# Kernel optimization log

Hardware: AMD Instinct MI355X
Metric: run time of the kernel (lower is better)

The kernel has to match this reference:

```python
import jax, jax.numpy as jnp
import numpy as np

B, S, D, H = 2, 2048, 1024, 8
DH = D // H          # hidden_dim == attn_dim == 128
TOTAL = 4 * D        # (2*hidden_dim + 2*attn_dim) * H
EPS = 1e-5
ROPE_BASE = 10000.0


def _layernorm(x, g, b):
    m = jnp.mean(x, axis=-1, keepdims=True)
    v = jnp.mean(jnp.square(x - m), axis=-1, keepdims=True)
    return (x - m) * jax.lax.rsqrt(v + EPS) * g + b


def _rope(x):
    # x: [B, H, S, DH], interleaved even/odd RoPE as in the torch module
    half = DH // 2
    inv_freq = 1.0 / (ROPE_BASE ** (jnp.arange(0, DH, 2, dtype=jnp.float32) / DH))  # [half]
    t = jnp.arange(x.shape[2], dtype=jnp.float32)
    freqs = t[:, None] * inv_freq[None, :]                 # [S, half]
    cos = jnp.cos(freqs)[None, None, :, :]                 # [1,1,S,half]
    sin = jnp.sin(freqs)[None, None, :, :]
    xe, xo = x[..., 0::2], x[..., 1::2]
    re = xe * cos - xo * sin
    ro = xe * sin + xo * cos
    return jnp.stack([re, ro], axis=-1).reshape(x.shape)


def setup_inputs() -> dict:
    key = jax.random.key(0)
    ks = jax.random.split(key, 6)
    x = jax.random.normal(ks[0], (B, S, D), dtype=jnp.float32)
    attention_mask = jnp.ones((B, S), dtype=bool)
    # weights stored [in, out] so forward is x @ W + b
    w_uvqk = 0.02 * jax.random.normal(ks[1], (D, TOTAL), dtype=jnp.float32)
    b_uvqk = jnp.zeros((TOTAL,), dtype=jnp.float32)
    w_out = 0.02 * jax.random.normal(ks[2], (3 * D, D), dtype=jnp.float32)
    b_out = jnp.zeros((D,), dtype=jnp.float32)
    ln1_g = jnp.ones((D,), dtype=jnp.float32)
    ln1_b = jnp.zeros((D,), dtype=jnp.float32)
    ln2_g = jnp.ones((D,), dtype=jnp.float32)
    ln2_b = jnp.zeros((D,), dtype=jnp.float32)
    return {"x": x, "attention_mask": attention_mask,
            "ln1_g": ln1_g, "ln1_b": ln1_b,
            "w_uvqk": w_uvqk, "b_uvqk": b_uvqk,
            "ln2_g": ln2_g, "ln2_b": ln2_b,
            "w_out": w_out, "b_out": b_out}


def reference(x, attention_mask, ln1_g, ln1_b, w_uvqk, b_uvqk, ln2_g, ln2_b, w_out, b_out):
    normed = _layernorm(x, ln1_g, ln1_b)
    uvqk = jax.nn.silu(normed @ w_uvqk + b_uvqk)          # [B,S,4D]
    u, v, q, k = jnp.split(uvqk, [D, 2 * D, 3 * D], axis=-1)
    q = q.reshape(B, S, H, DH).transpose(0, 2, 1, 3)      # [B,H,S,DH]
    k = k.reshape(B, S, H, DH).transpose(0, 2, 1, 3)
    v = v.reshape(B, S, H, DH).transpose(0, 2, 1, 3)
    q, k = _rope(q), _rope(k)
    scale = jnp.float32(DH) ** 0.5
    scores = jnp.einsum('bhsd,bhtd->bhst', q, k) / scale  # [B,H,S,S] fp32
    causal = jnp.tril(jnp.ones((S, S), dtype=bool))
    pad = attention_mask[:, None, :, None] & attention_mask[:, None, None, :]
    valid = pad & causal[None, None, :, :]
    scores = jnp.where(valid, scores, jnp.float32(-30.0))
    scores = jnp.clip(scores, -30.0, 30.0)
    attn = jax.nn.silu(scores)                            # SiLU instead of softmax
    ao = jnp.einsum('bhst,bhtd->bhsd', attn, v)           # [B,H,S,DH]
    ao = ao.transpose(0, 2, 1, 3).reshape(B, S, D)
    normed_attn = _layernorm(ao, ln2_g, ln2_b)
    cat = jnp.concatenate([u, ao, normed_attn * u], axis=-1)  # [B,S,3D]
    return x + (cat @ w_out + b_out)
```

## Files before the change

kernel.cpp:

```cpp
#include <hip/hip_runtime.h>
#include <hip/hip_bf16.h>
#include <math.h>

#define Bm 2
#define Sm 2048
#define Dm 1024
#define Hm 8
#define DHm 128
#define TOTALm 4096
#define ROWS (Bm*Sm)
#define K2m (3*Dm)

typedef __bf16 bf16;
typedef __bf16 bf16x8 __attribute__((ext_vector_type(8)));
typedef __bf16 bf16x4 __attribute__((ext_vector_type(4)));
typedef float  f32x4  __attribute__((ext_vector_type(4)));

__device__ __forceinline__ void stage_tile_128x32(
    const bf16* __restrict__ g, int ld, bf16* lds, int tid)
{
    int wid = tid >> 6;
    #pragma unroll
    for (int j = 0; j < 2; j++) {
        int e0  = (j*256 + tid) * 8;
        int row = e0 >> 5, col = e0 & 31;
        const bf16* src = g + (size_t)row*ld + col;
        bf16* dst = lds + (size_t)(j*256 + wid*64)*8;
        __builtin_amdgcn_global_load_lds(
            (const __attribute__((address_space(1))) unsigned int*)src,
            (__attribute__((address_space(3))) unsigned int*)dst,
            16, 0, 0);
    }
}

__device__ __forceinline__ void stage_tile_64x32(
    const bf16* __restrict__ g, int ld, bf16* lds, int tid)
{
    int wid = tid >> 6;
    int e0 = tid * 8;
    int row = e0 >> 5, col = e0 & 31;
    const bf16* src = g + (size_t)row*ld + col;
    bf16* dst = lds + (size_t)wid*512;
    __builtin_amdgcn_global_load_lds(
        (const __attribute__((address_space(1))) unsigned int*)src,
        (__attribute__((address_space(3))) unsigned int*)dst,
        16, 0, 0);
}

__global__ __launch_bounds__(256) void prep_kernel(
    const float* __restrict__ x, const float* __restrict__ g1,
    const float* __restrict__ b1, bf16* __restrict__ normed,
    const float* __restrict__ w_uvqk, bf16* __restrict__ Wt1,
    const float* __restrict__ w_out,  bf16* __restrict__ Wt2,
    float* __restrict__ ct, float* __restrict__ st)
{
    __shared__ float tile[32][33];
    __shared__ float red[4];
    __shared__ float stats[2];
    int bid = blockIdx.x;
    int tid = threadIdx.x;
    if (bid < 7168) {
        const float* in; bf16* out; int R, C, bx, by;
        if (bid < 4096) { in = w_uvqk; out = Wt1; R = Dm;  C = TOTALm; bx = bid & 127; by = bid >> 7; }
        else { int id2 = bid - 4096; in = w_out; out = Wt2; R = K2m; C = Dm; bx = id2 & 31; by = id2 >> 5; }
        int c0 = bx*32, r0 = by*32;
        int tx = tid & 31, ty = tid >> 5;
        for (int i=0;i<4;i++) {
            int r = ty + i*8;
            tile[r][tx] = in[(size_t)(r0+r)*C + c0+tx];
        }
        __syncthreads();
        for (int i=0;i<4;i++) {
            int cl = ty + i*8;
            out[(size_t)(c0+cl)*R + r0+tx] = (bf16)tile[tx][cl];
        }
    } else if (bid < 7680) {
        int idx = (bid - 7168)*256 + tid;
        int t = idx >> 6, p = idx & 63;
        float inv = expf(-0.143911568f * (float)p);
        float f = (float)t * inv;
        float sv, cv;
        sincosf(f, &sv, &cv);
        ct[idx] = cv; st[idx] = sv;
    } else {
        int row = bid - 7680;
        const float* xr = x + (size_t)row * Dm;
        float4 v = *(const float4*)(xr + tid*4);
        float s = v.x+v.y+v.z+v.w;
        for (int o=32;o>0;o>>=1) s += __shfl_down(s,o);
        int wid = tid>>6, lane = tid&63;
        if (lane==0) red[wid]=s;
        __syncthreads();
        if (tid==0) stats[0] = (red[0]+red[1]+red[2]+red[3]) * (1.f/Dm);
        __syncthreads();
        float m = stats[0];
        float d0=v.x-m,d1=v.y-m,d2=v.z-m,d3=v.w-m;
        float q = d0*d0+d1*d1+d2*d2+d3*d3;
        for (int o=32;o>0;o>>=1) q += __shfl_down(q,o);
        if (lane==0) red[wid]=q;
        __syncthreads();
        if (tid==0) stats[1] = rsqrtf((red[0]+red[1]+red[2]+red[3])*(1.f/Dm) + 1e-5f);
        __syncthreads();
        float rs = stats[1];
        float4 gv = *(const float4*)(g1 + tid*4);
        float4 bv = *(const float4*)(b1 + tid*4);
        bf16x4 o;
        o[0] = (bf16)(d0*rs*gv.x + bv.x);
        o[1] = (bf16)(d1*rs*gv.y + bv.y);
        o[2] = (bf16)(d2*rs*gv.z + bv.z);
        o[3] = (bf16)(d3*rs*gv.w + bv.w);
        *(bf16x4*)(normed + (size_t)row*Dm + tid*4) = o;
    }
}

__global__ __launch_bounds__(256,4) void gemm1_kernel(
    const bf16* __restrict__ A, const bf16* __restrict__ Bt,
    const float* __restrict__ bias,
    const float* __restrict__ ct, const float* __restrict__ st,
    bf16* __restrict__ cat, bf16* __restrict__ qb, bf16* __restrict__ kb,
    bf16* __restrict__ vt)
{
    __shared__ __align__(16) bf16 sm[17408];
    const int K = Dm;
    int m0 = blockIdx.y*128, n0 = blockIdx.x*128;
    int tid = threadIdx.x, wid = tid>>6, lane = tid&63;
    int quad = lane>>4, l16 = lane&15;
    int wm = (wid>>1)*64, wn = (wid&1)*64;
    f32x4 acc[4][4] = {};
    bf16* sA = sm;
    bf16* sB = sm + 8192;
    for (int k0=0;k0<K;k0+=64) {
        __syncthreads();
        stage_tile_128x32(A  + (size_t)m0*K + k0,      K, sA,        tid);
        stage_tile_128x32(A  + (size_t)m0*K + k0 + 32, K, sA + 4096, tid);
        stage_tile_128x32(Bt + (size_t)n0*K + k0,      K, sB,        tid);
        stage_tile_128x32(Bt + (size_t)n0*K + k0 + 32, K, sB + 4096, tid);
        __syncthreads();
        #pragma unroll
        for (int kc=0;kc<2;kc++) {
            bf16x8 af[4], bfr[4];
            #pragma unroll
            for (int t=0;t<4;t++) af[t]  = *(const bf16x8*)&sA[kc*4096 + (wm+t*16+l16)*32 + quad*8];
            #pragma unroll
            for (int t=0;t<4;t++) bfr[t] = *(const bf16x8*)&sB[kc*4096 + (wn+t*16+l16)*32 + quad*8];
            #pragma unroll
            for (int tm=0;tm<4;tm++)
                #pragma unroll
                for (int tn=0;tn<4;tn++)
                    acc[tm][tn] = __builtin_amdgcn_mfma_f32_16x16x32_bf16(af[tm], bfr[tn], acc[tm][tn], 0,0,0);
        }
    }
    int sect = n0 >> 10;
    if (sect == 1) {
        __syncthreads();
        #pragma unroll
        for (int tm=0;tm<4;tm++)
        #pragma unroll
        for (int tn=0;tn<4;tn++) {
            int colg = n0 + wn + tn*16 + l16;
            float bval = bias[colg];
            int d = colg & 127;
            #pragma unroll
            for (int r=0;r<4;r++) {
                int srow = wm + tm*16 + quad*4 + r;
                float val = acc[tm][tn][r] + bval;
                val = val / (1.f + __expf(-val));
                sm[d*136 + srow] = (bf16)val;
            }
        }
        __syncthreads();
        int h = (n0 >> 7) & 7;
        int b = m0 >> 11, s0l = m0 & 2047;
        int d2 = tid >> 1, sh = (tid & 1)*64;
        bf16* dst = vt + ((size_t)(b*Hm+h)*DHm + d2)*Sm + s0l + sh;
        const bf16* srcl = &sm[d2*136 + sh];
        #pragma unroll
        for (int i=0;i<8;i++)
            *(bf16x8*)(dst + i*8) = *(const bf16x8*)(srcl + i*8);
    } else if (sect == 0) {
        #pragma unroll
        for (int tm=0;tm<4;tm++)
        #pragma unroll
        for (int tn=0;tn<4;tn++) {
            int c = n0 + wn + tn*16 + l16;
            float bval = bias[c];
            #pragma unroll
            for (int r=0;r<4;r++) {
                int row = m0 + wm + tm*16 + quad*4 + r;
                float val = acc[tm][tn][r] + bval;
                val = val / (1.f + __expf(-val));
                cat[(size_t)row*K2m + c] = (bf16)val;
            }
        }
    } else {
        bf16* dstb = (sect==2) ? qb : kb;
        float postscale = (sect==2) ? 0.08838834764831845f : 1.0f;
        #pragma unroll
        for (int tm=0;tm<4;tm++)
        #pragma unroll
        for (int tn=0;tn<4;tn++) {
            int colg = n0 + wn + tn*16 + l16;
            int c = colg & 1023;
            int h = c>>7, d = c&127, p = d>>1;
            float bval = bias[colg];
            #pragma unroll
            for (int r=0;r<4;r++) {
                int row = m0 + wm + tm*16 + quad*4 + r;
                float val = acc[tm][tn][r] + bval;
                val = val / (1.f + __expf(-val));
                int b = row>>11, s = row&2047;
                float pv = __shfl_xor(val, 1);
                float cv = ct[s*64+p], sv = st[s*64+p];
                float res = (d&1) ? (pv*sv + val*cv) : (val*cv - pv*sv);
                dstb[((size_t)(b*Hm+h)*Sm + s)*DHm + d] = (bf16)(res * postscale);
            }
        }
    }
}

__global__ __launch_bounds__(256,3) void attn_kernel(
    const bf16* __restrict__ qb, const bf16* __restrict__ kb,
    const bf16* __restrict__ vt, float* __restrict__ ao0,
    float* __restrict__ ao1)
{
    __shared__ __align__(16) bf16 sK[16384];
    __shared__ __align__(16) bf16 P[64*136];
    int bid = blockIdx.x;
    int head = bid & 15;
    int idx = bid >> 4;
    int b = head >> 3, h = head & 7;
    int qt, k_begin, k_end;
    float* aoOut;
    if (idx < 32) {
        qt = 31 - (idx >> 1);
        int nkt = (qt >> 1) + 1;
        int half = (nkt + 1) >> 1;
        if ((idx & 1) == 0) { k_begin = 0;    k_end = half; aoOut = ao0; }
        else                { k_begin = half; k_end = nkt;  aoOut = ao1; }
    } else {
        qt = idx - 32;
        k_begin = 0; k_end = (qt >> 1) + 1;
        aoOut = ao0;
    }
    const size_t headoff = (size_t)(b*Hm+h)*Sm*DHm;
    const bf16* Q  = qb + headoff;
    const bf16* Km = kb + headoff;
    const bf16* V  = vt + headoff;
    int tid=threadIdx.x, wid=tid>>6, lane=tid&63, quad=lane>>4, l16=lane&15;
    int wm=(wid>>1)*32, wn=(wid&1)*64;
    int q0 = qt*64;
    f32x4 accO[2][4] = {};
    bf16x8 qf[4][2];
    #pragma unroll
    for (int kc=0;kc<4;kc++)
        #pragma unroll
        for (int t=0;t<2;t++)
            qf[kc][t] = *(const bf16x8*)(Q + (size_t)(q0+wm+t*16+l16)*DHm + kc*32 + quad*8);
    int e0 = tid*8, e1 = (256+tid)*8;
    int kr0 = e0>>5, kcol0 = e0&31;
    int kr1 = e1>>5, kcol1 = e1&31;
    int xorv = (tid>>3)&3;
    int sw0 = kr0*32 + (((tid&3)^xorv)<<3);
    int sw1 = sw0 + 2048;
    bf16x8 kreg[4][2];
    {
        int t0 = k_begin*128;
        #pragma unroll
        for (int kc=0;kc<4;kc++) {
            kreg[kc][0] = *(const bf16x8*)(Km + (size_t)(t0+kr0)*DHm + kc*32 + kcol0);
            kreg[kc][1] = *(const bf16x8*)(Km + (size_t)(t0+kr1)*DHm + kc*32 + kcol1);
        }
    }
    for (int kt=k_begin; kt<k_end; kt++) {
        int t0 = kt*128;
        __syncthreads();
        #pragma unroll
        for (int kc=0;kc<4;kc++) {
            *(bf16x8*)&sK[kc*4096 + sw0] = kreg[kc][0];
            *(bf16x8*)&sK[kc*4096 + sw1] = kreg[kc][1];
        }
        __syncthreads();
        if (kt+1 < k_end) {
            int t0n = t0 + 128;
            #pragma unroll
            for (int kc=0;kc<4;kc++) {
                kreg[kc][0] = *(const bf16x8*)(Km + (size_t)(t0n+kr0)*DHm + kc*32 + kcol0);
                kreg[kc][1] = *(const bf16x8*)(Km + (size_t)(t0n+kr1)*DHm + kc*32 + kcol1);
            }
        }
        bool clean = (t0 + 127 <= q0);
        #pragma unroll
        for (int ts=0; ts<4; ts++) {
            f32x4 accS[2] = {};
            int rr = wn + ts*16 + l16;
            int csw = (quad ^ ((rr>>1)&3))<<3;
            #pragma unroll
            for (int kc=0;kc<4;kc++) {
                bf16x8 bfr = *(const bf16x8*)&sK[kc*4096 + rr*32 + csw];
                #pragma unroll
                for (int tm=0;tm<2;tm++)
                    accS[tm] = __builtin_amdgcn_mfma_f32_16x16x32_bf16(qf[kc][tm], bfr, accS[tm], 0,0,0);
            }
            #pragma unroll
            for (int tm=0;tm<2;tm++)
                #pragma unroll
                for (int r=0;r<4;r++) {
                    int srow = wm+tm*16+quad*4+r;
                    float s = fminf(30.f, accS[tm][r]);
                    float p = s * __builtin_amdgcn_rcpf(1.f + __expf(-s));
                    if (!clean && (t0+rr > q0+srow)) p = 0.f;
                    P[srow*136 + rr] = (bf16)p;
                }
        }
        __syncthreads();
        int kcn = ((q0 + 63 - t0) >> 5) + 1;
        if (kcn > 4) kcn = 4;
        for (int kc=0;kc<kcn;kc++) {
            bf16x8 af[2], bfr[4];
            #pragma unroll
            for (int t=0;t<2;t++) af[t]  = *(const bf16x8*)&P[(wm+t*16+l16)*136 + kc*32 + quad*8];
            #pragma unroll
            for (int t=0;t<4;t++) bfr[t] = *(const bf16x8*)(V + (size_t)(wn+t*16+l16)*Sm + t0 + kc*32 + quad*8);
            #pragma unroll
            for (int tm=0;tm<2;tm++)
                #pragma unroll
                for (int tn=0;tn<4;tn++)
                    accO[tm][tn] = __builtin_amdgcn_mfma_f32_16x16x32_bf16(af[tm], bfr[tn], accO[tm][tn], 0,0,0);
        }
    }
    #pragma unroll
    for (int tm=0;tm<2;tm++)
    #pragma unroll
    for (int tn=0;tn<4;tn++)
        #pragma unroll
        for (int r=0;r<4;r++) {
            int s = q0+wm+tm*16+quad*4+r;
            int d = wn+tn*16+l16;
            aoOut[((size_t)(b*Sm+s))*Dm + h*DHm + d] = accO[tm][tn][r];
        }
}

__global__ __launch_bounds__(256) void ln2_cat_kernel(
    const float* __restrict__ ao0, const float* __restrict__ ao1,
    const float* __restrict__ g,
    const float* __restrict__ bb, bf16* __restrict__ cat)
{
    int row = blockIdx.x;
    int tid = threadIdx.x;
    int s = row & 2047;
    float4 v  = *(const float4*)(ao0 + (size_t)row*Dm + tid*4);
    if (s >= 1024) {
        float4 v1 = *(const float4*)(ao1 + (size_t)row*Dm + tid*4);
        v.x += v1.x; v.y += v1.y; v.z += v1.z; v.w += v1.w;
    }
    float ssum = v.x+v.y+v.z+v.w;
    for (int o=32;o>0;o>>=1) ssum += __shfl_down(ssum,o);
    __shared__ float red[4]; __shared__ float stats[2];
    int wid = tid>>6, lane = tid&63;
    if (lane==0) red[wid]=ssum;
    __syncthreads();
    if (tid==0) stats[0] = (red[0]+red[1]+red[2]+red[3]) * (1.f/Dm);
    __syncthreads();
    float m = stats[0];
    float d0=v.x-m,d1=v.y-m,d2=v.z-m,d3=v.w-m;
    float q = d0*d0+d1*d1+d2*d2+d3*d3;
    for (int o=32;o>0;o>>=1) q += __shfl_down(q,o);
    if (lane==0) red[wid]=q;
    __syncthreads();
    if (tid==0) stats[1] = rsqrtf((red[0]+red[1]+red[2]+red[3])*(1.f/Dm) + 1e-5f);
    __syncthreads();
    float rs = stats[1];
    float4 gv = *(const float4*)(g + tid*4);
    float4 bv = *(const float4*)(bb + tid*4);
    bf16* crow = cat + (size_t)row * K2m;
    bf16x4 u4 = *(const bf16x4*)(crow + tid*4);
    bf16x4 a4, nu4;
    a4[0]=(bf16)v.x; a4[1]=(bf16)v.y; a4[2]=(bf16)v.z; a4[3]=(bf16)v.w;
    nu4[0]=(bf16)(((v.x-m)*rs*gv.x+bv.x) * (float)u4[0]);
    nu4[1]=(bf16)(((v.y-m)*rs*gv.y+bv.y) * (float)u4[1]);
    nu4[2]=(bf16)(((v.z-m)*rs*gv.z+bv.z) * (float)u4[2]);
    nu4[3]=(bf16)(((v.w-m)*rs*gv.w+bv.w) * (float)u4[3]);
    *(bf16x4*)(crow + 1024 + tid*4) = a4;
    *(bf16x4*)(crow + 2048 + tid*4) = nu4;
}

__global__ __launch_bounds__(256,4) void gemm2_kernel(
    const bf16* __restrict__ A, const bf16* __restrict__ Bt,
    const float* __restrict__ bias, const float* __restrict__ x,
    float* __restrict__ out)
{
    __shared__ __align__(16) bf16 sm[12288];
    const int K = K2m, N = Dm;
    int m0 = blockIdx.y*128, n0 = blockIdx.x*64;
    int tid = threadIdx.x, wid = tid>>6, lane = tid&63;
    int quad = lane>>4, l16 = lane&15;
    int wm = (wid>>1)*64, wn = (wid&1)*32;
    f32x4 acc[4][2] = {};
    bf16* sA = sm;
    bf16* sB = sm + 8192;
    for (int k0=0;k0<K;k0+=64) {
        __syncthreads();
        stage_tile_128x32(A  + (size_t)m0*K + k0,      K, sA,        tid);
        stage_tile_128x32(A  + (size_t)m0*K + k0 + 32, K, sA + 4096, tid);
        stage_tile_64x32 (Bt + (size_t)n0*K + k0,      K, sB,        tid);
        stage_tile_64x32 (Bt + (size_t)n0*K + k0 + 32, K, sB + 2048, tid);
        __syncthreads();
        #pragma unroll
        for (int kc=0;kc<2;kc++) {
            bf16x8 af[4], bfr[2];
            #pragma unroll
            for (int t=0;t<4;t++) af[t]  = *(const bf16x8*)&sA[kc*4096 + (wm+t*16+l16)*32 + quad*8];
            #pragma unroll
            for (int t=0;t<2;t++) bfr[t] = *(const bf16x8*)&sB[kc*2048 + (wn+t*16+l16)*32 + quad*8];
            #pragma unroll
            for (int tm=0;tm<4;tm++)
                #pragma unroll
                for (int tn=0;tn<2;tn++)
                    acc[tm][tn] = __builtin_amdgcn_mfma_f32_16x16x32_bf16(af[tm], bfr[tn], acc[tm][tn], 0,0,0);
        }
    }
    #pragma unroll
    for (int tm=0;tm<4;tm++)
    #pragma unroll
    for (int tn=0;tn<2;tn++) {
        int col = n0 + wn + tn*16 + l16;
        float bval = bias[col];
        #pragma unroll
        for (int r=0;r<4;r++) {
            int row = m0 + wm + tm*16 + quad*4 + r;
            out[(size_t)row*N + col] = acc[tm][tn][r] + bval + x[(size_t)row*N + col];
        }
    }
}

extern "C" void kernel_launch(void* const* d_in, const int* in_sizes, int n_in,
                              void* d_out, int out_size, void* d_ws, size_t ws_size,
                              hipStream_t stream)
{
    const float* x      = (const float*)d_in[0];
    const float* ln1_g  = (const float*)d_in[2];
    const float* ln1_b  = (const float*)d_in[3];
    const float* w_uvqk = (const float*)d_in[4];
    const float* b_uvqk = (const float*)d_in[5];
    const float* ln2_g  = (const float*)d_in[6];
    const float* ln2_b  = (const float*)d_in[7];
    const float* w_out  = (const float*)d_in[8];
    const float* b_out  = (const float*)d_in[9];

    char* w = (char*)d_ws;
    bf16*  normed = (bf16*)(w);
    bf16*  Wt1    = (bf16*)(w + 8388608);
    bf16*  Wt2    = (bf16*)(w + 16777216);
    bf16*  qb     = (bf16*)(w + 23068672);
    bf16*  kb     = (bf16*)(w + 31457280);
    bf16*  vt     = (bf16*)(w + 39845888);
    float* ao0    = (float*)(w + 48234496);
    bf16*  cat    = (bf16*)(w + 65011712);
    float* ct     = (float*)(w + 90177536);
    float* st     = (float*)(w + 90701824);
    float* ao1    = (float*)(w);

    prep_kernel<<<11776, 256, 0, stream>>>(x, ln1_g, ln1_b, normed,
                                           w_uvqk, Wt1, w_out, Wt2, ct, st);
    gemm1_kernel<<<dim3(TOTALm/128, ROWS/128), 256, 0, stream>>>(
        normed, Wt1, b_uvqk, ct, st, cat, qb, kb, vt);
    attn_kernel<<<768, 256, 0, stream>>>(qb, kb, vt, ao0, ao1);
    ln2_cat_kernel<<<ROWS, 256, 0, stream>>>(ao0, ao1, ln2_g, ln2_b, cat);
    gemm2_kernel<<<dim3(Dm/64, ROWS/128), 256, 0, stream>>>(
        cat, Wt2, b_out, x, (float*)d_out);
}
```

Baseline: 256.1 us.

## Restructure gemm1 into 256x256 tiles with double-buffered swizzled LDS pipeline

Rewrites the first GEMM to use 512-thread blocks computing 256x256 output tiles with 64-wide K steps. Global-to-LDS loads are double-buffered two stages ahead and overlap the MFMA work, and the LDS layout is XOR-swizzled to avoid bank conflicts. MFMA phases are interleaved with fragment loads and raised wave priority. The aim is to raise arithmetic intensity and hide memory latency, at the cost of much more LDS per block (about 132KB), more registers, and only 256 blocks on the GPU, which may leave some CUs idle.

```diff
diff --git a/kernel.cpp b/kernel.cpp
--- a/kernel.cpp
+++ b/kernel.cpp
@@ -45,6 +45,29 @@
         (const __attribute__((address_space(1))) unsigned int*)src,
         (__attribute__((address_space(3))) unsigned int*)dst,
         16, 0, 0);
+}
+
+__device__ __forceinline__ void g1_stage_half(
+    const bf16* __restrict__ g, int ldg, bf16* lds, int tid)
+{
+    int wid = tid >> 6;
+    #pragma unroll
+    for (int j = 0; j < 2; j++) {
+        int idx = j*512 + tid;
+        int row = idx >> 3, ch = idx & 7;
+        int sch = ch ^ (row & 7);
+        const bf16* src = g + (size_t)row*ldg + sch*8;
+        bf16* dst = lds + (size_t)(j*512 + wid*64)*8;
+        __builtin_amdgcn_global_load_lds(
+            (const __attribute__((address_space(1))) unsigned int*)src,
+            (__attribute__((address_space(3))) unsigned int*)dst,
+            16, 0, 0);
+    }
+}
+
+__device__ __forceinline__ bf16x8 g1_ld(const bf16* s, int row, int kk, int quad)
+{
+    return *(const bf16x8*)&s[(row<<6) + ((((kk<<2)|quad) ^ (row & 7))<<3)];
 }
 
 __global__ __launch_bounds__(256) void prep_kernel(
@@ -113,81 +136,162 @@
     }
 }
 
-__global__ __launch_bounds__(256,4) void gemm1_kernel(
+__global__ __launch_bounds__(512,2) void gemm1_kernel(
     const bf16* __restrict__ A, const bf16* __restrict__ Bt,
     const float* __restrict__ bias,
     const float* __restrict__ ct, const float* __restrict__ st,
     bf16* __restrict__ cat, bf16* __restrict__ qb, bf16* __restrict__ kb,
     bf16* __restrict__ vt)
 {
-    __shared__ __align__(16) bf16 sm[17408];
+    __shared__ __align__(16) bf16 smem[67584];
     const int K = Dm;
-    int m0 = blockIdx.y*128, n0 = blockIdx.x*128;
-    int tid = threadIdx.x, wid = tid>>6, lane = tid&63;
+    int m0 = blockIdx.y*256, n0 = blockIdx.x*256;
+    int tid = threadIdx.x, lane = tid&63;
+    int wid = tid>>6;
     int quad = lane>>4, l16 = lane&15;
-    int wm = (wid>>1)*64, wn = (wid&1)*64;
-    f32x4 acc[4][4] = {};
-    bf16* sA = sm;
-    bf16* sB = sm + 8192;
-    for (int k0=0;k0<K;k0+=64) {
-        __syncthreads();
-        stage_tile_128x32(A  + (size_t)m0*K + k0,      K, sA,        tid);
-        stage_tile_128x32(A  + (size_t)m0*K + k0 + 32, K, sA + 4096, tid);
-        stage_tile_128x32(Bt + (size_t)n0*K + k0,      K, sB,        tid);
-        stage_tile_128x32(Bt + (size_t)n0*K + k0 + 32, K, sB + 4096, tid);
-        __syncthreads();
-        #pragma unroll
-        for (int kc=0;kc<2;kc++) {
-            bf16x8 af[4], bfr[4];
-            #pragma unroll
-            for (int t=0;t<4;t++) af[t]  = *(const bf16x8*)&sA[kc*4096 + (wm+t*16+l16)*32 + quad*8];
-            #pragma unroll
-            for (int t=0;t<4;t++) bfr[t] = *(const bf16x8*)&sB[kc*4096 + (wn+t*16+l16)*32 + quad*8];
-            #pragma unroll
-            for (int tm=0;tm<4;tm++)
-                #pragma unroll
-                for (int tn=0;tn<4;tn++)
-                    acc[tm][tn] = __builtin_amdgcn_mfma_f32_16x16x32_bf16(af[tm], bfr[tn], acc[tm][tn], 0,0,0);
-        }
-    }
+    int wr = (wid>>2)*128, wc = (wid&3)*64;
+    f32x4 acc[8][4] = {};
+    bf16* sA0 = smem;
+    bf16* sB0 = smem + 32768;
+
+    #pragma unroll
+    for (int t0=0; t0<2; t0++) {
+        bf16* sAp = sA0 + t0*16384;
+        bf16* sBp = sB0 + t0*16384;
+        const bf16* Ab = A  + (size_t)m0*K + t0*64;
+        const bf16* Bb = Bt + (size_t)n0*K + t0*64;
+        g1_stage_half(Ab,           K, sAp,        tid);
+        g1_stage_half(Ab + 128*K,   K, sAp + 8192, tid);
+        g1_stage_half(Bb,           K, sBp,        tid);
+        g1_stage_half(Bb + 128*K,   K, sBp + 8192, tid);
+    }
+
+    for (int t=0; t<16; ++t) {
+        int p = t & 1;
+        bf16* sAp = sA0 + p*16384;
+        bf16* sBp = sB0 + p*16384;
+        asm volatile("s_waitcnt vmcnt(8)" ::: "memory");
+        __builtin_amdgcn_s_barrier();
+        bf16x8 a0[4][2], a1[4][2], b0[2][2], b1[2][2];
+        #pragma unroll
+        for (int mf=0; mf<4; mf++) {
+            int row = wr + mf*16 + l16;
+            a0[mf][0] = g1_ld(sAp, row, 0, quad);
+            a0[mf][1] = g1_ld(sAp, row, 1, quad);
+        }
+        #pragma unroll
+        for (int nf=0; nf<2; nf++) {
+            int row = wc + nf*16 + l16;
+            b0[nf][0] = g1_ld(sBp, row, 0, quad);
+            b0[nf][1] = g1_ld(sBp, row, 1, quad);
+        }
+        asm volatile("s_waitcnt lgkmcnt(0)" ::: "memory");
+        __builtin_amdgcn_s_setprio(1);
+        #pragma unroll
+        for (int mf=0; mf<4; mf++)
+            #pragma unroll
+            for (int nf=0; nf<2; nf++)
+                #pragma unroll
+                for (int kk=0; kk<2; kk++)
+                    acc[mf][nf] = __builtin_amdgcn_mfma_f32_16x16x32_bf16(a0[mf][kk], b0[nf][kk], acc[mf][nf], 0,0,0);
+        __builtin_amdgcn_s_setprio(0);
+        __builtin_amdgcn_s_barrier();
+        #pragma unroll
+        for (int nf=0; nf<2; nf++) {
+            int row = wc + (nf+2)*16 + l16;
+            b1[nf][0] = g1_ld(sBp, row, 0, quad);
+            b1[nf][1] = g1_ld(sBp, row, 1, quad);
+        }
+        asm volatile("s_waitcnt lgkmcnt(0)" ::: "memory");
+        __builtin_amdgcn_s_setprio(1);
+        #pragma unroll
+        for (int mf=0; mf<4; mf++)
+            #pragma unroll
+            for (int nf=0; nf<2; nf++)
+                #pragma unroll
+                for (int kk=0; kk<2; kk++)
+                    acc[mf][nf+2] = __builtin_amdgcn_mfma_f32_16x16x32_bf16(a0[mf][kk], b1[nf][kk], acc[mf][nf+2], 0,0,0);
+        __builtin_amdgcn_s_setprio(0);
+        __builtin_amdgcn_s_barrier();
+        #pragma unroll
+        for (int mf=0; mf<4; mf++) {
+            int row = wr + (mf+4)*16 + l16;
+            a1[mf][0] = g1_ld(sAp, row, 0, quad);
+            a1[mf][1] = g1_ld(sAp, row, 1, quad);
+        }
+        asm volatile("s_waitcnt lgkmcnt(0)" ::: "memory");
+        __builtin_amdgcn_s_setprio(1);
+        #pragma unroll
+        for (int mf=0; mf<4; mf++)
+            #pragma unroll
+            for (int nf=0; nf<2; nf++)
+                #pragma unroll
+                for (int kk=0; kk<2; kk++)
+                    acc[mf+4][nf+2] = __builtin_amdgcn_mfma_f32_16x16x32_bf16(a1[mf][kk], b1[nf][kk], acc[mf+4][nf+2], 0,0,0);
+        __builtin_amdgcn_s_setprio(0);
+        __builtin_amdgcn_s_barrier();
+        __builtin_amdgcn_s_setprio(1);
+        #pragma unroll
+        for (int mf=0; mf<4; mf++)
+            #pragma unroll
+            for (int nf=0; nf<2; nf++)
+                #pragma unroll
+                for (int kk=0; kk<2; kk++)
+                    acc[mf+4][nf] = __builtin_amdgcn_mfma_f32_16x16x32_bf16(a1[mf][kk], b0[nf][kk], acc[mf+4][nf], 0,0,0);
+        __builtin_amdgcn_s_setprio(0);
+        __builtin_amdgcn_s_barrier();
+        if (t < 15) {
+            int tn = (t+2) & 15;
+            const bf16* Ab = A  + (size_t)m0*K + tn*64;
+            const bf16* Bb = Bt + (size_t)n0*K + tn*64;
+            g1_stage_half(Ab,           K, sAp,        tid);
+            g1_stage_half(Ab + 128*K,   K, sAp + 8192, tid);
+            g1_stage_half(Bb,           K, sBp,        tid);
+            g1_stage_half(Bb + 128*K,   K, sBp + 8192, tid);
+        }
+    }
+    asm volatile("s_waitcnt vmcnt(0)" ::: "memory");
+
     int sect = n0 >> 10;
     if (sect == 1) {
         __syncthreads();
-        #pragma unroll
-        for (int tm=0;tm<4;tm++)
-        #pragma unroll
-        for (int tn=0;tn<4;tn++) {
-            int colg = n0 + wn + tn*16 + l16;
-            float bval = bias[colg];
-            int d = colg & 127;
+        bf16* vb = smem;
+        #pragma unroll
+        for (int mf=0; mf<8; mf++)
+        #pragma unroll
+        for (int nf=0; nf<4; nf++) {
+            int colin = wc + nf*16 + l16;
+            int hh = colin >> 7, d = colin & 127;
+            float bval = bias[n0 + colin];
             #pragma unroll
             for (int r=0;r<4;r++) {
-                int srow = wm + tm*16 + quad*4 + r;
-                float val = acc[tm][tn][r] + bval;
+                int srow = wr + mf*16 + quad*4 + r;
+                float val = acc[mf][nf][r] + bval;
                 val = val / (1.f + __expf(-val));
-                sm[d*136 + srow] = (bf16)val;
+                vb[(d*2 + hh)*264 + srow] = (bf16)val;
             }
         }
         __syncthreads();
-        int h = (n0 >> 7) & 7;
         int b = m0 >> 11, s0l = m0 & 2047;
-        int d2 = tid >> 1, sh = (tid & 1)*64;
-        bf16* dst = vt + ((size_t)(b*Hm+h)*DHm + d2)*Sm + s0l + sh;
-        const bf16* srcl = &sm[d2*136 + sh];
-        #pragma unroll
-        for (int i=0;i<8;i++)
+        int hh = tid >> 8, rest = tid & 255;
+        int d = rest >> 1, sh = (rest & 1)*128;
+        int h = ((n0 >> 7) + hh) & 7;
+        bf16* dst = vt + ((size_t)(b*Hm+h)*DHm + d)*Sm + s0l + sh;
+        const bf16* srcl = &vb[(d*2 + hh)*264 + sh];
+        #pragma unroll
+        for (int i=0;i<16;i++)
             *(bf16x8*)(dst + i*8) = *(const bf16x8*)(srcl + i*8);
     } else if (sect == 0) {
         #pragma unroll
-        for (int tm=0;tm<4;tm++)
-        #pragma unroll
-        for (int tn=0;tn<4;tn++) {
-            int c = n0 + wn + tn*16 + l16;
+        for (int mf=0; mf<8; mf++)
+        #pragma unroll
+        for (int nf=0; nf<4; nf++) {
+            int c = n0 + wc + nf*16 + l16;
             float bval = bias[c];
             #pragma unroll
             for (int r=0;r<4;r++) {
-                int row = m0 + wm + tm*16 + quad*4 + r;
-                float val = acc[tm][tn][r] + bval;
+                int row = m0 + wr + mf*16 + quad*4 + r;
+                float val = acc[mf][nf][r] + bval;
                 val = val / (1.f + __expf(-val));
                 cat[(size_t)row*K2m + c] = (bf16)val;
             }
@@ -196,21 +300,21 @@
         bf16* dstb = (sect==2) ? qb : kb;
         float postscale = (sect==2) ? 0.08838834764831845f : 1.0f;
         #pragma unroll
-        for (int tm=0;tm<4;tm++)
-        #pragma unroll
-        for (int tn=0;tn<4;tn++) {
-            int colg = n0 + wn + tn*16 + l16;
+        for (int mf=0; mf<8; mf++)
+        #pragma unroll
+        for (int nf=0; nf<4; nf++) {
+            int colg = n0 + wc + nf*16 + l16;
             int c = colg & 1023;
-            int h = c>>7, d = c&127, p = d>>1;
+            int h = c>>7, d = c&127, pp = d>>1;
             float bval = bias[colg];
             #pragma unroll
             for (int r=0;r<4;r++) {
-                int row = m0 + wm + tm*16 + quad*4 + r;
-                float val = acc[tm][tn][r] + bval;
+                int row = m0 + wr + mf*16 + quad*4 + r;
+                float val = acc[mf][nf][r] + bval;
                 val = val / (1.f + __expf(-val));
                 int b = row>>11, s = row&2047;
                 float pv = __shfl_xor(val, 1);
-                float cv = ct[s*64+p], sv = st[s*64+p];
+                float cv = ct[s*64+pp], sv = st[s*64+pp];
                 float res = (d&1) ? (pv*sv + val*cv) : (val*cv - pv*sv);
                 dstb[((size_t)(b*Hm+h)*Sm + s)*DHm + d] = (bf16)(res * postscale);
             }
@@ -462,7 +566,7 @@
 
     prep_kernel<<<11776, 256, 0, stream>>>(x, ln1_g, ln1_b, normed,
                                            w_uvqk, Wt1, w_out, Wt2, ct, st);
-    gemm1_kernel<<<dim3(TOTALm/128, ROWS/128), 256, 0, stream>>>(
+    gemm1_kernel<<<dim3(16, 16), 512, 0, stream>>>(
         normed, Wt1, b_uvqk, ct, st, cat, qb, kb, vt);
     attn_kernel<<<768, 256, 0, stream>>>(qb, kb, vt, ao0, ao1);
     ln2_cat_kernel<<<ROWS, 256, 0, stream>>>(ao0, ao1, ln2_g, ln2_b, cat);
```

Measured after the change: 257.9 us. Within noise of the previous version (+0.7%).
